# Performance work log

Hardware: AMD Instinct MI355X
Metric: run time of the kernel (lower is better)

The kernel has to match this reference:

```python
import jax, jax.numpy as jnp
import numpy as np

B, N_HEADS, D_MODEL, S = 4, 16, 128, 2048
SQRT_D = np.sqrt(D_MODEL).astype(np.float32)


def setup_inputs() -> dict:
    key = jax.random.key(0)
    kx, kq, kk, kv, kw = jax.random.split(key, 5)
    N = B * N_HEADS
    return {
        "x": jax.random.normal(kx, (B, D_MODEL, S), dtype=jnp.float32),
        "Q": jax.random.normal(kq, (N, D_MODEL, S), dtype=jnp.float32),
        "K": jax.random.normal(kk, (N, D_MODEL, S), dtype=jnp.float32),
        "V": jax.random.normal(kv, (N, D_MODEL, S), dtype=jnp.float32),
        "W": jax.random.normal(kw, (N_HEADS * D_MODEL, D_MODEL), dtype=jnp.float32) * 0.02,
    }


def reference(x, Q, K, V, W):
    # x contributes only its shape (the repeated copy is overwritten in the original)
    b, d_model, s = x.shape
    # scores[n, i, j] = sum_d Q[n, d, i] * K[n, d, j] / sqrt(d_model)
    scores = jnp.einsum("ndi,ndj->nij", Q, K) / SQRT_D  # [N, S, S]
    # legacy F.softmax (no dim) on a 3D tensor -> softmax over dim=1 (query index)
    attn = jax.nn.softmax(scores, axis=1)
    # out[n, d, j] = sum_i V[n, d, i] * attn[n, i, j]
    out = jnp.einsum("ndi,nij->ndj", V, attn)  # [N, d_model, S]
    out = out.reshape(b, N_HEADS * d_model, s)  # [B, H*d_model, S]
    # final projection: W^T @ out, W: [H*d_model, d_model]
    return jnp.einsum("hd,bhs->bds", W, out)  # [B, d_model, S]
```

## Files before the change

### kernel.cpp

```cpp
#include <hip/hip_runtime.h>
#include <hip/hip_bf16.h>

typedef unsigned short u16;
typedef unsigned int   u32;
typedef short  short8v __attribute__((ext_vector_type(8)));
typedef u16    u16x8   __attribute__((ext_vector_type(8)));
typedef float  f32x16  __attribute__((ext_vector_type(16)));
typedef float  f32x4v  __attribute__((ext_vector_type(4)));
typedef u32    u32x2   __attribute__((ext_vector_type(2)));
typedef u32    u32x4   __attribute__((ext_vector_type(4)));

#define HEADS 64
#define DMODEL 128
#define SEQ 2048

#define SCQ 0.1275293f
#define PSTR 80


__device__ __forceinline__ f32x16 mfma_bf16(short8v a, short8v b, f32x16 c) {
  return __builtin_amdgcn_mfma_f32_32x32x16_bf16(a, b, c, 0, 0, 0);
}

__device__ __forceinline__ f32x16 fzero16() {
  f32x16 z;
#pragma unroll
  for (int i = 0; i < 16; ++i) z[i] = 0.f;
  return z;
}

__device__ __forceinline__ float fast_exp2(float x) {
  float r;
  asm("v_exp_f32 %0, %1" : "=v"(r) : "v"(x));
  return r;
}

__device__ __forceinline__ u32 bfround(float x) {
  u32 u = __builtin_bit_cast(u32, x);
  u += 0x7fffu + ((u >> 16) & 1u);
  return u >> 16;
}
__device__ __forceinline__ u32 bfpair(float lo, float hi) {
  u32 a = __builtin_bit_cast(u32, lo); a += 0x7fffu + ((a >> 16) & 1u);
  u32 b = __builtin_bit_cast(u32, hi); b += 0x7fffu + ((b >> 16) & 1u);
  return (a >> 16) | (b & 0xffff0000u);
}
__device__ __forceinline__ u32 packbf(float lo, float hi) {
  u32 l16 = (u32)__builtin_bit_cast(u16, __float2bfloat16(lo));
  u32 h16 = (u32)__builtin_bit_cast(u16, __float2bfloat16(hi));
  return l16 | (h16 << 16);
}

typedef const __attribute__((address_space(1))) void* gp1_t;
typedef __attribute__((address_space(3))) void* lp3_t;
__device__ __forceinline__ void gload16(const u16* g, u16* l) {
  __builtin_amdgcn_global_load_lds((gp1_t)g, (lp3_t)l, 16, 0, 0);
}

__device__ __forceinline__ void stage_T(const float* __restrict__ src, int pos0,
                                        u16* lds, int tid) {
  int ic = tid & 7;
  int d0 = (tid >> 3) * 2;
  const float* p = src + d0 * SEQ + pos0 + ic * 8;
  f32x4v xa = *reinterpret_cast<const f32x4v*>(p);
  f32x4v xb = *reinterpret_cast<const f32x4v*>(p + 4);
  f32x4v ya = *reinterpret_cast<const f32x4v*>(p + SEQ);
  f32x4v yb = *reinterpret_cast<const f32x4v*>(p + SEQ + 4);
  u32* lds32 = reinterpret_cast<u32*>(lds);
  int cc = d0 >> 3;
#pragma unroll
  for (int k = 0; k < 8; ++k) {
    int r = ic * 8 + k;
    int c2 = cc ^ (r & 15);
    float xv = (k < 4) ? xa[k & 3] : xb[k & 3];
    float yv = (k < 4) ? ya[k & 3] : yb[k & 3];
    lds32[(r * 128 + c2 * 8 + (d0 & 7)) >> 1] = bfpair(xv, yv);
  }
}

__device__ __forceinline__ short8v ld_at(const u16* lds, int row, int chunk) {
  return *reinterpret_cast<const short8v*>(lds + row * 128 + ((chunk ^ (row & 15)) * 8));
}
__device__ __forceinline__ short8v ld_vt(const u16* lds, int d, int chunk) {
  return *reinterpret_cast<const short8v*>(lds + d * 64 + ((chunk ^ (d & 7)) * 8));
}

__global__ __launch_bounds__(256) void prep_kernel(
    const float* __restrict__ Q, const float* __restrict__ V,
    const float* __restrict__ Wsrc, u16* __restrict__ Qt,
    u16* __restrict__ V16t, u16* __restrict__ Wt) {
  int blk = blockIdx.x;
  int t = threadIdx.x;
  if (blk < 2048) {
    int n = blk >> 5, pt = blk & 31;
    const float* src = Q + (size_t)n * DMODEL * SEQ;
    u16* dst = Qt + (size_t)n * SEQ * DMODEL + (size_t)pt * 64 * DMODEL;
    int pq = t & 15, dq = t >> 4;
#pragma unroll
    for (int p = 0; p < 2; ++p) {
      int d0 = (dq + 16 * p) * 4;
      const float* s0 = src + (size_t)d0 * SEQ + pt * 64 + pq * 4;
      f32x4v r0 = *reinterpret_cast<const f32x4v*>(s0);
      f32x4v r1 = *reinterpret_cast<const f32x4v*>(s0 + SEQ);
      f32x4v r2 = *reinterpret_cast<const f32x4v*>(s0 + 2 * SEQ);
      f32x4v r3 = *reinterpret_cast<const f32x4v*>(s0 + 3 * SEQ);
#pragma unroll
      for (int j = 0; j < 4; ++j) {
        u32x2 v = { bfpair(r0[j] * SCQ, r1[j] * SCQ), bfpair(r2[j] * SCQ, r3[j] * SCQ) };
        *reinterpret_cast<u32x2*>(dst + (pq * 4 + j) * DMODEL + d0) = v;
      }
    }
  } else if (blk < 4096) {
    int b2 = blk - 2048;
    int n = b2 >> 5, it = b2 & 31;
    int s8 = (t & 7) * 8;
    const float* src = V + (size_t)n * DMODEL * SEQ + it * 64 + s8;
    u16* dst = V16t + (size_t)b2 * DMODEL * 64 + s8;
#pragma unroll
    for (int rr = 0; rr < 4; ++rr) {
      int d = (t >> 3) + 32 * rr;
      const float* p = src + (size_t)d * SEQ;
      f32x4v a = *reinterpret_cast<const f32x4v*>(p);
      f32x4v b = *reinterpret_cast<const f32x4v*>(p + 4);
      u32x4 v = { bfpair(a[0], a[1]), bfpair(a[2], a[3]),
                  bfpair(b[0], b[1]), bfpair(b[2], b[3]) };
      *reinterpret_cast<u32x4*>(dst + d * 64) = v;
    }
  } else {
    int e = (blk - 4096) * 256 + t;
#pragma unroll
    for (int rr = 0; rr < 2; ++rr) {
      int o = e + rr * 131072;
      int dm = o >> 11, c = o & 2047;
      Wt[o] = (u16)bfround(Wsrc[c * 128 + dm]);
    }
  }
}

__global__ __launch_bounds__(1024, 4) void attn_kernel(
    const u16* __restrict__ Qt, const float* __restrict__ K,
    const u16* __restrict__ V16t, u16* __restrict__ Ows) {
  __shared__ __align__(16) u16 AT2[2][64 * DMODEL];
  __shared__ __align__(16) u16 VT2[2][DMODEL * 64];
  __shared__ __align__(16) u16 PB[2][256 * PSTR];
  __shared__ float AL[2][256];
  __shared__ float LL[256];
  const int tid = threadIdx.x;
  const int w = tid >> 6;
  const int lane = tid & 63;
  const int g = lane >> 5;
  const int lj = lane & 31;
  const int p_ = blockIdx.x;
  const int n = ((p_ >> 6) << 3) | (p_ & 7);
  const int j0 = ((p_ >> 3) & 7) * 256;
  const u16* Qtn = Qt + (size_t)n * SEQ * DMODEL;
  const float* Kb = K + (size_t)n * DMODEL * SEQ;
  const u16* Vtn = V16t + (size_t)n * 32 * DMODEL * 64;

  int qoff[2], voff[2];
#pragma unroll
  for (int i = 0; i < 2; ++i) {
    int idx = (w & 7) * 2 + i;
    int pos = idx * 4 + (lane >> 4);
    qoff[i] = pos * DMODEL + (((lane & 15) ^ (pos & 15)) * 8);
    int d = idx * 8 + (lane >> 3);
    voff[i] = d * 64 + (((lane & 7) ^ (d & 7)) * 8);
  }

  if (w < 8) {
    const u16* qb = Qtn;
#pragma unroll
    for (int i = 0; i < 2; ++i)
      gload16(qb + qoff[i], AT2[0] + ((w & 7) * 2 + i) * 512);
  }
  short8v bq[8];
  u16* KS = PB[0];
#pragma unroll 1
  for (int p = 0; p < 4; ++p) {
    if (tid < 512) stage_T(Kb, j0 + p * 64, KS, tid);
    __syncthreads();
    if (w < 8 && (w >> 1) == p) {
      int row = (w & 1) * 32 + lj;
#pragma unroll
      for (int c = 0; c < 8; ++c) bq[c] = ld_at(KS, row, 2 * c + g);
    }
    __syncthreads();
  }

  if (w < 8) {
    float m_run = -1e30f, l_run = 0.f;
    const int prow = w * 32 + lj;
    u16* const prowbase0 = PB[0] + prow * PSTR;
    u16* const prowbase1 = PB[1] + prow * PSTR;
    const int swz = prow & 7;

#pragma unroll 1
    for (int t = 0; t <= 32; ++t) {
      if (t < 32) {
        const u16* qb = Qtn + (size_t)((t + 1) & 31) * (64 * DMODEL);
        u16* ab = AT2[(t + 1) & 1];
#pragma unroll
        for (int i = 0; i < 2; ++i)
          gload16(qb + qoff[i], ab + ((w & 7) * 2 + i) * 512);

        const u16* curAT = AT2[t & 1];
        f32x16 c0 = fzero16(), c1 = fzero16();
        __builtin_amdgcn_s_setprio(1);
#pragma unroll
        for (int dc = 0; dc < 8; ++dc) {
          short8v a0 = ld_at(curAT, lj, 2 * dc + g);
          short8v a1 = ld_at(curAT, 32 + lj, 2 * dc + g);
          c0 = mfma_bf16(a0, bq[dc], c0);
          c1 = mfma_bf16(a1, bq[dc], c1);
        }
        __builtin_amdgcn_s_setprio(0);

        float m8[8];
#pragma unroll
        for (int r = 0; r < 8; ++r)
          m8[r] = fmaxf(fmaxf(c0[r], c0[r + 8]), fmaxf(c1[r], c1[r + 8]));
#pragma unroll
        for (int r = 0; r < 4; ++r) m8[r] = fmaxf(m8[r], m8[r + 4]);
        float mx = fmaxf(fmaxf(m8[0], m8[1]), fmaxf(m8[2], m8[3]));
        mx = fmaxf(mx, __shfl_xor(mx, 32, 64));

        float al = 1.0f;
        if (!__all(mx <= m_run + 8.f)) {
          float mn = fmaxf(m_run, mx);
          al = fast_exp2(m_run - mn);
          m_run = mn;
          l_run *= al;
        }
        if (!g) AL[t & 1][prow] = al;

#pragma unroll
        for (int r = 0; r < 16; ++r) c0[r] = fast_exp2(c0[r] - m_run);
#pragma unroll
        for (int r = 0; r < 16; ++r) c1[r] = fast_exp2(c1[r] - m_run);
        float s8[8];
#pragma unroll
        for (int r = 0; r < 8; ++r) s8[r] = (c0[r] + c0[r + 8]) + (c1[r] + c1[r + 8]);
#pragma unroll
        for (int r = 0; r < 4; ++r) s8[r] += s8[r + 4];
        float ps = (s8[0] + s8[1]) + (s8[2] + s8[3]);
        ps += __shfl_xor(ps, 32, 64);
        l_run += ps;

        u16* pdst = (t & 1) ? prowbase1 : prowbase0;
#pragma unroll
        for (int half = 0; half < 2; ++half) {
#pragma unroll
          for (int q = 0; q < 4; ++q) {
            u32x2 val;
            val.x = half ? packbf(c1[4 * q + 0], c1[4 * q + 1])
                         : packbf(c0[4 * q + 0], c0[4 * q + 1]);
            val.y = half ? packbf(c1[4 * q + 2], c1[4 * q + 3])
                         : packbf(c0[4 * q + 2], c0[4 * q + 3]);
            int G = q + 4 * half;
            *reinterpret_cast<u32x2*>(pdst + ((G ^ swz) << 3) + 4 * g) = val;
          }
        }
      }
      __syncthreads();
    }
    if (!g) LL[prow] = l_run;
    __syncthreads();
  } else {
    f32x16 oa0 = fzero16(), oa1 = fzero16(), ob0 = fzero16(), ob1 = fzero16();
    const int cw = w - 8;
    const int ju = cw & 3, dh = cw >> 2;
    const int ja = 64 * ju + lj;
    const int jb = ja + 32;
    const int swza = ja & 7, swzb = jb & 7;
    const int dbase = dh * 64;

#pragma unroll 1
    for (int t = 0; t <= 32; ++t) {
      if (t < 32) {
        const u16* vb = Vtn + (size_t)t * (DMODEL * 64);
        u16* vbuf = VT2[t & 1];
#pragma unroll
        for (int i = 0; i < 2; ++i)
          gload16(vb + voff[i], vbuf + (cw * 2 + i) * 512);
      }
      if (t >= 1) {
        const int tp = t - 1;
        const u16* curVT = VT2[tp & 1];
        const u16* pa = PB[tp & 1] + ja * PSTR;
        const u16* pb = PB[tp & 1] + jb * PSTR;
        float ala = AL[tp & 1][ja];
        float alb = AL[tp & 1][jb];
        if (!__all((ala == 1.0f) && (alb == 1.0f))) {
#pragma unroll
          for (int r = 0; r < 16; ++r) {
            oa0[r] *= ala; oa1[r] *= ala; ob0[r] *= alb; ob1[r] *= alb;
          }
        }
        __builtin_amdgcn_s_setprio(1);
#pragma unroll
        for (int kc = 0; kc < 4; ++kc) {
          int G = 2 * kc + g;
          short8v pfa = *reinterpret_cast<const short8v*>(pa + ((G ^ swza) << 3));
          short8v pfb = *reinterpret_cast<const short8v*>(pb + ((G ^ swzb) << 3));
          short8v v0 = ld_vt(curVT, dbase + lj, G);
          short8v v1 = ld_vt(curVT, dbase + 32 + lj, G);
          oa0 = mfma_bf16(v0, pfa, oa0);
          oa1 = mfma_bf16(v1, pfa, oa1);
          ob0 = mfma_bf16(v0, pfb, ob0);
          ob1 = mfma_bf16(v1, pfb, ob1);
        }
        __builtin_amdgcn_s_setprio(0);
      }
      __syncthreads();
    }
    __syncthreads();
    float inva = 1.f / LL[ja];
    float invb = 1.f / LL[jb];
    u16* obase_a = Ows + ((size_t)n * SEQ + j0 + ja) * DMODEL;
    u16* obase_b = Ows + ((size_t)n * SEQ + j0 + jb) * DMODEL;
#define STORE_OT(OV, OB, DT, INV)                                         \
    {                                                                     \
      _Pragma("unroll") for (int q = 0; q < 4; ++q) {                     \
        int d0 = dbase + (DT) * 32 + 4 * g + 8 * q;                       \
        u32x2 val;                                                        \
        val.x = bfpair(OV[4 * q + 0] * (INV), OV[4 * q + 1] * (INV));     \
        val.y = bfpair(OV[4 * q + 2] * (INV), OV[4 * q + 3] * (INV));     \
        *reinterpret_cast<u32x2*>((OB) + d0) = val;                       \
      }                                                                   \
    }
    STORE_OT(oa0, obase_a, 0, inva) STORE_OT(oa1, obase_a, 1, inva)
    STORE_OT(ob0, obase_b, 0, invb) STORE_OT(ob1, obase_b, 1, invb)
#undef STORE_OT
  }
}

__global__ __launch_bounds__(256) void proj_kernel(
    const u16* __restrict__ Ows, const u16* __restrict__ Wt, float* __restrict__ out) {
  __shared__ __align__(16) u16 BT[32 * 128];
  const int tid = threadIdx.x;
  const int w = tid >> 6, lane = tid & 63, g = lane >> 5, lj = lane & 31;
  const int b = blockIdx.x >> 6;
  const int j0 = (blockIdx.x & 63) * 32;
  f32x16 acc = fzero16();
#pragma unroll 1
  for (int h = 0; h < 16; ++h) {
    __syncthreads();
#pragma unroll
    for (int rr = 0; rr < 2; ++rr) {
      int s = tid + rr * 256;
      int r = s >> 4, cc = s & 15;
      u16x8 v = *reinterpret_cast<const u16x8*>(
          Ows + ((size_t)(b * 16 + h) * SEQ + j0 + r) * DMODEL + cc * 8);
      *reinterpret_cast<u16x8*>(BT + r * 128 + ((cc ^ (r & 7)) * 8)) = v;
    }
    __syncthreads();
#pragma unroll
    for (int kc = 0; kc < 8; ++kc) {
      short8v a = *reinterpret_cast<const short8v*>(
          Wt + (size_t)(w * 32 + lj) * SEQ + h * 128 + kc * 16 + g * 8);
      short8v bb = *reinterpret_cast<const short8v*>(
          BT + lj * 128 + (((2 * kc + g) ^ (lj & 7)) * 8));
      acc = mfma_bf16(a, bb, acc);
    }
  }
#pragma unroll
  for (int q = 0; q < 4; ++q) {
#pragma unroll
    for (int r = 0; r < 4; ++r) {
      int dm = w * 32 + 4 * g + 8 * q + r;
      out[((size_t)b * DMODEL + dm) * SEQ + j0 + lj] = acc[4 * q + r];
    }
  }
}

extern "C" void kernel_launch(void* const* d_in, const int* in_sizes, int n_in,
                              void* d_out, int out_size, void* d_ws, size_t ws_size,
                              hipStream_t stream) {
  (void)in_sizes; (void)n_in; (void)out_size; (void)ws_size;
  const float* Q = (const float*)d_in[1];
  const float* K = (const float*)d_in[2];
  const float* V = (const float*)d_in[3];
  const float* W = (const float*)d_in[4];
  const size_t NEL = (size_t)HEADS * SEQ * DMODEL;
  u16* Qt   = (u16*)d_ws;
  u16* V16t = Qt + NEL;
  u16* Ows  = V16t + NEL;
  u16* Wt   = Ows + NEL;
  float* out = (float*)d_out;

  prep_kernel<<<dim3(4608), dim3(256), 0, stream>>>(Q, V, W, Qt, V16t, Wt);
  attn_kernel<<<dim3(512), dim3(1024), 0, stream>>>(Qt, K, V16t, Ows);
  proj_kernel<<<dim3(256), dim3(256), 0, stream>>>(Ows, Wt, out);
}
```

Before: 234.2 us.

## Load V fragments directly from global in MFMA-ready layout, drop V LDS staging

The prep kernel now writes V in bf16 with a layout where each lane's 8-element MFMA operand is contiguous, grouped by k-chunk. The attention kernel's PV warps read their V fragments straight from global memory (L2) into registers each step, and the double-buffered VT2 shared-memory tile and its async copies are removed. This frees LDS and removes the staged copy plus the LDS reads for V. The cost is global-load latency inside the loop, since nothing is prefetched a step ahead, and each V tile is fetched by several warps without sharing through LDS.

Result: slower. 247.1 us (+5.5%).

```diff
diff --git a/kernel.cpp b/kernel.cpp
--- a/kernel.cpp
+++ b/kernel.cpp
@@ -81,9 +81,6 @@
 __device__ __forceinline__ short8v ld_at(const u16* lds, int row, int chunk) {
   return *reinterpret_cast<const short8v*>(lds + row * 128 + ((chunk ^ (row & 15)) * 8));
 }
-__device__ __forceinline__ short8v ld_vt(const u16* lds, int d, int chunk) {
-  return *reinterpret_cast<const short8v*>(lds + d * 64 + ((chunk ^ (d & 7)) * 8));
-}
 
 __global__ __launch_bounds__(256) void prep_kernel(
     const float* __restrict__ Q, const float* __restrict__ V,
@@ -113,18 +110,16 @@
   } else if (blk < 4096) {
     int b2 = blk - 2048;
     int n = b2 >> 5, it = b2 & 31;
-    int s8 = (t & 7) * 8;
-    const float* src = V + (size_t)n * DMODEL * SEQ + it * 64 + s8;
-    u16* dst = V16t + (size_t)b2 * DMODEL * 64 + s8;
-#pragma unroll
-    for (int rr = 0; rr < 4; ++rr) {
-      int d = (t >> 3) + 32 * rr;
-      const float* p = src + (size_t)d * SEQ;
-      f32x4v a = *reinterpret_cast<const f32x4v*>(p);
-      f32x4v b = *reinterpret_cast<const f32x4v*>(p + 4);
+    int d = t & 127, h = t >> 7;
+    const float* src = V + ((size_t)n * DMODEL + d) * SEQ + it * 64 + h * 32;
+    u16* dst = V16t + ((size_t)b2 * 8 + h * 4) * 1024 + d * 8;
+#pragma unroll
+    for (int gg = 0; gg < 4; ++gg) {
+      f32x4v a = *reinterpret_cast<const f32x4v*>(src + gg * 8);
+      f32x4v b = *reinterpret_cast<const f32x4v*>(src + gg * 8 + 4);
       u32x4 v = { bfpair(a[0], a[1]), bfpair(a[2], a[3]),
                   bfpair(b[0], b[1]), bfpair(b[2], b[3]) };
-      *reinterpret_cast<u32x4*>(dst + d * 64) = v;
+      *reinterpret_cast<u32x4*>(dst + gg * 1024) = v;
     }
   } else {
     int e = (blk - 4096) * 256 + t;
@@ -141,7 +136,6 @@
     const u16* __restrict__ Qt, const float* __restrict__ K,
     const u16* __restrict__ V16t, u16* __restrict__ Ows) {
   __shared__ __align__(16) u16 AT2[2][64 * DMODEL];
-  __shared__ __align__(16) u16 VT2[2][DMODEL * 64];
   __shared__ __align__(16) u16 PB[2][256 * PSTR];
   __shared__ float AL[2][256];
   __shared__ float LL[256];
@@ -155,16 +149,14 @@
   const int j0 = ((p_ >> 3) & 7) * 256;
   const u16* Qtn = Qt + (size_t)n * SEQ * DMODEL;
   const float* Kb = K + (size_t)n * DMODEL * SEQ;
-  const u16* Vtn = V16t + (size_t)n * 32 * DMODEL * 64;
-
-  int qoff[2], voff[2];
+  const u16* Vtn = V16t + (size_t)n * 32 * 8192;
+
+  int qoff[2];
 #pragma unroll
   for (int i = 0; i < 2; ++i) {
     int idx = (w & 7) * 2 + i;
     int pos = idx * 4 + (lane >> 4);
     qoff[i] = pos * DMODEL + (((lane & 15) ^ (pos & 15)) * 8);
-    int d = idx * 8 + (lane >> 3);
-    voff[i] = d * 64 + (((lane & 7) ^ (d & 7)) * 8);
   }
 
   if (w < 8) {
@@ -273,19 +265,19 @@
     const int jb = ja + 32;
     const int swza = ja & 7, swzb = jb & 7;
     const int dbase = dh * 64;
+    const int vlane = g * 1024 + (dbase + lj) * 8;
 
 #pragma unroll 1
     for (int t = 0; t <= 32; ++t) {
-      if (t < 32) {
-        const u16* vb = Vtn + (size_t)t * (DMODEL * 64);
-        u16* vbuf = VT2[t & 1];
-#pragma unroll
-        for (int i = 0; i < 2; ++i)
-          gload16(vb + voff[i], vbuf + (cw * 2 + i) * 512);
-      }
       if (t >= 1) {
         const int tp = t - 1;
-        const u16* curVT = VT2[tp & 1];
+        const u16* vt = Vtn + (size_t)tp * 8192;
+        short8v vf[8];
+#pragma unroll
+        for (int kc = 0; kc < 4; ++kc) {
+          vf[2 * kc]     = *reinterpret_cast<const short8v*>(vt + kc * 2048 + vlane);
+          vf[2 * kc + 1] = *reinterpret_cast<const short8v*>(vt + kc * 2048 + vlane + 256);
+        }
         const u16* pa = PB[tp & 1] + ja * PSTR;
         const u16* pb = PB[tp & 1] + jb * PSTR;
         float ala = AL[tp & 1][ja];
@@ -302,12 +294,10 @@
           int G = 2 * kc + g;
           short8v pfa = *reinterpret_cast<const short8v*>(pa + ((G ^ swza) << 3));
           short8v pfb = *reinterpret_cast<const short8v*>(pb + ((G ^ swzb) << 3));
-          short8v v0 = ld_vt(curVT, dbase + lj, G);
-          short8v v1 = ld_vt(curVT, dbase + 32 + lj, G);
-          oa0 = mfma_bf16(v0, pfa, oa0);
-          oa1 = mfma_bf16(v1, pfa, oa1);
-          ob0 = mfma_bf16(v0, pfb, ob0);
-          ob1 = mfma_bf16(v1, pfb, ob1);
+          oa0 = mfma_bf16(vf[2 * kc],     pfa, oa0);
+          oa1 = mfma_bf16(vf[2 * kc + 1], pfa, oa1);
+          ob0 = mfma_bf16(vf[2 * kc],     pfb, ob0);
+          ob1 = mfma_bf16(vf[2 * kc + 1], pfb, ob1);
         }
         __builtin_amdgcn_s_setprio(0);
       }
```
